# Kernel optimization log

Measured on AMD Instinct MI355X. Metric: run time of the kernel, lower is better.

Reference implementation:

```python
import jax, jax.numpy as jnp
import numpy as np

D_MODEL = 768
N_HEADS = 8
HEAD_DIM = D_MODEL // N_HEADS
B, S, A = 8, 8192, 512


def setup_inputs() -> dict:
    key = jax.random.key(0)
    ks = jax.random.split(key, 12)
    hidden_states = jax.random.normal(ks[0], (B, S, D_MODEL), dtype=jnp.float32)
    # unique anchors per batch element (scatter with duplicates is ill-defined)
    anchor_indices = jax.vmap(lambda k: jax.random.permutation(k, S)[:A])(
        jax.random.split(ks[1], B)).astype(jnp.int64)
    std = 1.0 / np.sqrt(D_MODEL)
    def lin(kw, kb):
        w = jax.random.uniform(kw, (D_MODEL, D_MODEL), jnp.float32, -std, std)
        b = jax.random.uniform(kb, (D_MODEL,), jnp.float32, -std, std)
        return w, b
    wq, bq = lin(ks[2], ks[3])
    wk, bk = lin(ks[4], ks[5])
    wv, bv = lin(ks[6], ks[7])
    wo, bo = lin(ks[8], ks[9])
    ln_g = jnp.ones((D_MODEL,), jnp.float32)
    ln_b = jnp.zeros((D_MODEL,), jnp.float32)
    return dict(hidden_states=hidden_states, anchor_indices=anchor_indices,
                ln_g=ln_g, ln_b=ln_b, wq=wq, bq=bq, wk=wk, bk=bk,
                wv=wv, bv=bv, wo=wo, bo=bo)


def reference(hidden_states, anchor_indices, ln_g, ln_b, wq, bq, wk, bk, wv, bv, wo, bo):
    batch, seq_len, d_model = hidden_states.shape
    n_anchors = anchor_indices.shape[1]
    # gather anchor tokens: (B, A, D)
    anchor_hidden = jnp.take_along_axis(hidden_states, anchor_indices[..., None], axis=1)
    # LayerNorm (eps=1e-5, matching nn.LayerNorm default)
    mu = jnp.mean(anchor_hidden, axis=-1, keepdims=True)
    var = jnp.var(anchor_hidden, axis=-1, keepdims=True)
    x = (anchor_hidden - mu) * jax.lax.rsqrt(var + 1e-5) * ln_g + ln_b
    # QKV projections -> (B, H, A, Hd)
    def heads(y):
        return y.reshape(batch, n_anchors, N_HEADS, HEAD_DIM).transpose(0, 2, 1, 3)
    q = heads(x @ wq.T + bq)
    k = heads(x @ wk.T + bk)
    v = heads(x @ wv.T + bv)
    scale = 1.0 / np.sqrt(HEAD_DIM)
    scores = jnp.einsum('bhad,bhed->bhae', q, k) * scale  # (B,H,A,A)
    attn = jax.nn.softmax(scores, axis=-1)  # dropout is identity in eval
    out = jnp.einsum('bhae,bhed->bhad', attn, v)
    out = out.transpose(0, 2, 1, 3).reshape(batch, n_anchors, d_model)
    out = out @ wo.T + bo
    # scatter back into zeros at anchor positions
    batch_idx = jnp.arange(batch)[:, None]
    output = jnp.zeros_like(hidden_states).at[batch_idx, anchor_indices].set(out)
    return output
```

## Files before the change

kernel.cpp:

```cpp
#include <hip/hip_runtime.h>

#define DM 768
#define NHEAD 8
#define HDIM 96
#define NB 8
#define SEQ 8192
#define NA 512
#define MROW (NB*NA)
#define NQKV (3*DM)
#define QBLK 32
#define FILLB 512

typedef __attribute__((ext_vector_type(4))) float f32x4;
typedef __attribute__((ext_vector_type(8))) short s16x8;

static __device__ __forceinline__ unsigned short f2bf(float x) {
  unsigned int u = __float_as_uint(x);
  u += 0x7fffu + ((u >> 16) & 1u);
  return (unsigned short)(u >> 16);
}
static __device__ __forceinline__ float bf2f(unsigned short h) {
  return __uint_as_float(((unsigned int)h) << 16);
}

static __device__ __forceinline__ void gld_lds16(const void* g, void* l) {
  __builtin_amdgcn_global_load_lds(
      (const __attribute__((address_space(1))) unsigned int*)g,
      (__attribute__((address_space(3))) unsigned int*)l, 16, 0, 0);
}

__global__ __launch_bounds__(256) void prologue(
    const float* __restrict__ hs, const int* __restrict__ anc,
    const float* __restrict__ gam, const float* __restrict__ bet,
    const float* __restrict__ wq, const float* __restrict__ wk,
    const float* __restrict__ wv, const float* __restrict__ wo,
    unsigned short* __restrict__ xh,
    unsigned short* __restrict__ w1h, unsigned short* __restrict__ woh)
{
  __shared__ float red[8];
  const int bid = blockIdx.x;
  const int t = threadIdx.x;
  if (bid < MROW) {
    int r = bid;
    int b = r >> 9, a = r & (NA - 1);
    int idx = anc[b * NA + a];
    const float* src = hs + ((size_t)b * SEQ + idx) * DM;
    float e0 = src[t], e1 = src[t + 256], e2 = src[t + 512];
    float s = e0 + e1 + e2;
    float ss = e0*e0 + e1*e1 + e2*e2;
    #pragma unroll
    for (int o = 1; o < 64; o <<= 1) { s += __shfl_xor(s, o); ss += __shfl_xor(ss, o); }
    int w = t >> 6, lane = t & 63;
    if (lane == 0) { red[w] = s; red[4 + w] = ss; }
    __syncthreads();
    s  = red[0] + red[1] + red[2] + red[3];
    ss = red[4] + red[5] + red[6] + red[7];
    float mu = s * (1.f / DM);
    float var = ss * (1.f / DM) - mu * mu;
    float rstd = rsqrtf(var + 1e-5f);
    size_t base = (size_t)r * DM;
    #pragma unroll
    for (int p = 0; p < 3; ++p) {
      int c = t + p * 256;
      float e = (p == 0) ? e0 : (p == 1) ? e1 : e2;
      float y = (e - mu) * rstd * gam[c] + bet[c];
      xh[base + c] = f2bf(y);
    }
  } else {
    const int i = (bid - MROW) * 256 + t;
    const int T1_4 = (NQKV * DM) / 4;
    const int TW_4 = (DM * DM) / 4;
    float4 v;
    unsigned short* dh; int e4;
    if (i < T1_4) {
      v = (i < TW_4) ? reinterpret_cast<const float4*>(wq)[i]
        : (i < 2*TW_4) ? reinterpret_cast<const float4*>(wk)[i - TW_4]
                       : reinterpret_cast<const float4*>(wv)[i - 2*TW_4];
      dh = w1h; e4 = i;
    } else {
      int j = i - T1_4;
      v = reinterpret_cast<const float4*>(wo)[j];
      dh = woh; e4 = j;
    }
    uint2 ph;
    ph.x = (unsigned)f2bf(v.x) | ((unsigned)f2bf(v.y) << 16);
    ph.y = (unsigned)f2bf(v.z) | ((unsigned)f2bf(v.w) << 16);
    reinterpret_cast<uint2*>(dh)[e4] = ph;
  }
}

template<int EPI>
__global__ __launch_bounds__(256, 4) void gemm128(
    const unsigned short* __restrict__ Ah,
    const unsigned short* __restrict__ Bh,
    const float* __restrict__ biasq, const float* __restrict__ biask, const float* __restrict__ biasv,
    unsigned short* __restrict__ qh,
    unsigned short* __restrict__ kh,
    unsigned short* __restrict__ vh,
    const float* __restrict__ biaso, const int* __restrict__ anc,
    float* __restrict__ outp,
    f32x4* __restrict__ fillp, int n4, int nCompute, int gcols)
{
  __shared__ unsigned short sA[128 * 64], sB[128 * 64];
  const int bidx = blockIdx.x;
  if (bidx >= nCompute) {
    const f32x4 z = {0.f, 0.f, 0.f, 0.f};
    int i = (bidx - nCompute) * 256 + threadIdx.x;
    for (; i < n4; i += FILLB * 256) __builtin_nontemporal_store(z, fillp + i);
    return;
  }
  const int tid = threadIdx.x, lane = tid & 63, w = tid >> 6;
  const int wr = w >> 1, wc = w & 1;
  const unsigned int wg = ((unsigned)bidx & 7) * ((unsigned)nCompute >> 3) + ((unsigned)bidx >> 3);
  const int m0 = (int)(wg / gcols) * 128, n0 = (int)(wg % gcols) * 128;
  const int rsel = lane & 15, kg = lane >> 4;
  f32x4 acc[4][4] = {};

  for (int k0 = 0; k0 < DM; k0 += 64) {
    __syncthreads();
    #pragma unroll
    for (int c = 0; c < 4; ++c) {
      const int gg = w * 256 + c * 64;
      const int g = gg + lane;
      const int row = g >> 3, slot = g & 7;
      const int kk = k0 + ((slot ^ (row & 7)) << 3);
      gld_lds16(Ah + (size_t)(m0 + row) * DM + kk, sA + gg * 8);
      gld_lds16(Bh + (size_t)(n0 + row) * DM + kk, sB + gg * 8);
    }
    __syncthreads();
    #pragma unroll
    for (int s = 0; s < 2; ++s) {
      s16x8 af[4], bf[4];
      #pragma unroll
      for (int i = 0; i < 4; ++i) {
        const int row = wr * 64 + i * 16 + rsel;
        const int as = (((s << 2) | kg) ^ (row & 7));
        af[i] = *reinterpret_cast<const s16x8*>(sA + row * 64 + as * 8);
        const int col = wc * 64 + i * 16 + rsel;
        const int bs = (((s << 2) | kg) ^ (col & 7));
        bf[i] = *reinterpret_cast<const s16x8*>(sB + col * 64 + bs * 8);
      }
      #pragma unroll
      for (int i = 0; i < 4; ++i)
        #pragma unroll
        for (int j = 0; j < 4; ++j)
          acc[i][j] = __builtin_amdgcn_mfma_f32_16x16x32_bf16(af[i], bf[j], acc[i][j], 0, 0, 0);
    }
  }

  #pragma unroll
  for (int i = 0; i < 4; ++i)
    #pragma unroll
    for (int j = 0; j < 4; ++j)
      #pragma unroll
      for (int r = 0; r < 4; ++r) {
        const int row = m0 + wr * 64 + i * 16 + kg * 4 + r;
        const int col = n0 + wc * 64 + j * 16 + rsel;
        const float v = acc[i][j][r];
        const int b = row >> 9, a = row & (NA - 1);
        if (EPI == 1) {
          const int sec = (col >= 2 * DM) ? 2 : (col >= DM ? 1 : 0);
          const int f = col - sec * DM;
          const int hh = f / HDIM, d = f - hh * HDIM;
          const float* bp = (sec == 0) ? biasq : (sec == 1) ? biask : biasv;
          const float val = v + bp[f];
          const int bhh = b * NHEAD + hh;
          if (sec == 0) {
            const size_t o = ((size_t)bhh * NA + a) * HDIM + d; qh[o] = f2bf(val);
          } else if (sec == 1) {
            const size_t o = ((size_t)bhh * NA + a) * HDIM + d; kh[o] = f2bf(val);
          } else {
            const size_t o = ((size_t)bhh * HDIM + d) * NA + a; vh[o] = f2bf(val);
          }
        } else {
          const int sidx = anc[b * NA + a];
          outp[((size_t)b * SEQ + sidx) * DM + col] = v + biaso[col];
        }
      }
}

__global__ __launch_bounds__(512, 4) void attn_fused(
    const unsigned short* __restrict__ qh,
    const unsigned short* __restrict__ kh,
    const unsigned short* __restrict__ vh,
    unsigned short* __restrict__ oh)
{
  __shared__ unsigned int S[QBLK * 512];
  __shared__ float rsum_lds[QBLK];
  const int blk = blockIdx.x;
  const int xcd = blk & 7, slot = blk >> 3;
  const int qt = slot & 15, bh = (slot >> 4) * 8 + xcd;
  const int b = bh >> 3, h = bh & 7;
  const int tid = threadIdx.x, lane = tid & 63, w = tid >> 6;
  const int rt = w & 1, ctq = w >> 1;
  const int rsel = lane & 15, kg = lane >> 4;
  const int q0 = qt * QBLK;

  s16x8 qf[3];
  {
    const size_t qrow = (size_t)bh * NA + q0 + rt * 16 + rsel;
    const unsigned short* qp = qh + qrow * HDIM + kg * 8;
    #pragma unroll
    for (int kc = 0; kc < 3; ++kc)
      qf[kc] = *reinterpret_cast<const s16x8*>(qp + kc * 32);
  }
  const float scale = 0.10206207261596575f;
  const unsigned short* kb_h = kh + (size_t)bh * NA * HDIM;

  for (int ct2 = 0; ct2 < 8; ++ct2) {
    const int ct = ctq * 8 + ct2;
    f32x4 acc = {0.f, 0.f, 0.f, 0.f};
    const unsigned short* kp = kb_h + (size_t)(ct * 16 + rsel) * HDIM + kg * 8;
    #pragma unroll
    for (int kc = 0; kc < 3; ++kc) {
      s16x8 kfh = *reinterpret_cast<const s16x8*>(kp + kc * 32);
      __builtin_amdgcn_s_setprio(1);
      acc = __builtin_amdgcn_mfma_f32_16x16x32_bf16(qf[kc], kfh, acc, 0, 0, 0);
      __builtin_amdgcn_s_setprio(0);
    }
    #pragma unroll
    for (int r = 0; r < 4; ++r) {
      int row = rt * 16 + kg * 4 + r;
      int col = ct * 16 + rsel;
      S[row * 512 + (col ^ ((row & 7) << 2))] = __float_as_uint(acc[r] * scale);
    }
  }
  __syncthreads();

  {
    const int row = w * 4 + (lane >> 4);
    const int sub = lane & 15;
    const int srow = (row & 7) << 2;
    unsigned int* rowp = &S[row * 512];
    float mx = -3.0e38f;
    #pragma unroll 8
    for (int i = 0; i < 8; ++i) {
      int c = sub * 4 + i * 64;
      uint4 u = *reinterpret_cast<const uint4*>(rowp + (c ^ srow));
      mx = fmaxf(mx, fmaxf(fmaxf(__uint_as_float(u.x), __uint_as_float(u.y)),
                           fmaxf(__uint_as_float(u.z), __uint_as_float(u.w))));
    }
    mx = fmaxf(mx, __shfl_xor(mx, 1));
    mx = fmaxf(mx, __shfl_xor(mx, 2));
    mx = fmaxf(mx, __shfl_xor(mx, 4));
    mx = fmaxf(mx, __shfl_xor(mx, 8));
    float sum = 0.f;
    #pragma unroll 8
    for (int i = 0; i < 8; ++i) {
      int c = sub * 4 + i * 64;
      uint4 u = *reinterpret_cast<const uint4*>(rowp + (c ^ srow));
      float p0 = __expf(__uint_as_float(u.x) - mx);
      float p1 = __expf(__uint_as_float(u.y) - mx);
      float p2 = __expf(__uint_as_float(u.z) - mx);
      float p3 = __expf(__uint_as_float(u.w) - mx);
      sum += p0 + p1 + p2 + p3;
      uint4 pk;
      pk.x = ((unsigned)f2bf(p0)) << 16;
      pk.y = ((unsigned)f2bf(p1)) << 16;
      pk.z = ((unsigned)f2bf(p2)) << 16;
      pk.w = ((unsigned)f2bf(p3)) << 16;
      *reinterpret_cast<uint4*>(rowp + (c ^ srow)) = pk;
    }
    sum += __shfl_xor(sum, 1);
    sum += __shfl_xor(sum, 2);
    sum += __shfl_xor(sum, 4);
    sum += __shfl_xor(sum, 8);
    if (sub == 0) rsum_lds[row] = 1.f / sum;
  }
  __syncthreads();

  const unsigned short* vb_h = vh + (size_t)bh * HDIM * NA;
  for (int task = w; task < 12; task += 8) {
    const int nt = task % 6, rt2 = task / 6;
    f32x4 acc = {0.f, 0.f, 0.f, 0.f};
    const int row = rt2 * 16 + rsel;
    const int srow = (row & 7) << 2;
    const unsigned int* rowp = &S[row * 512];
    for (int kc = 0; kc < 16; ++kc) {
      int c = kc * 32 + kg * 8;
      uint4 ua = *reinterpret_cast<const uint4*>(rowp + ((c) ^ srow));
      uint4 ub = *reinterpret_cast<const uint4*>(rowp + ((c + 4) ^ srow));
      s16x8 ph;
      ph[0] = (short)(ua.x >> 16); ph[1] = (short)(ua.y >> 16);
      ph[2] = (short)(ua.z >> 16); ph[3] = (short)(ua.w >> 16);
      ph[4] = (short)(ub.x >> 16); ph[5] = (short)(ub.y >> 16);
      ph[6] = (short)(ub.z >> 16); ph[7] = (short)(ub.w >> 16);
      const unsigned short* vp = vb_h + (size_t)(nt * 16 + rsel) * NA + c;
      s16x8 vfh = *reinterpret_cast<const s16x8*>(vp);
      __builtin_amdgcn_s_setprio(1);
      acc = __builtin_amdgcn_mfma_f32_16x16x32_bf16(ph, vfh, acc, 0, 0, 0);
      __builtin_amdgcn_s_setprio(0);
    }
    #pragma unroll
    for (int r = 0; r < 4; ++r) {
      const float rinv = rsum_lds[rt2 * 16 + kg * 4 + r];
      const int rowg = b * NA + q0 + rt2 * 16 + kg * 4 + r;
      size_t o = (size_t)rowg * DM + h * HDIM + nt * 16 + rsel;
      oh[o] = f2bf(acc[r] * rinv);
    }
  }
}

extern "C" void kernel_launch(void* const* d_in, const int* in_sizes, int n_in,
                              void* d_out, int out_size, void* d_ws, size_t ws_size,
                              hipStream_t stream)
{
  const float* hs   = (const float*)d_in[0];
  const int*   anc  = (const int*)d_in[1];
  const float* ln_g = (const float*)d_in[2];
  const float* ln_b = (const float*)d_in[3];
  const float* wq = (const float*)d_in[4];
  const float* bq = (const float*)d_in[5];
  const float* wk = (const float*)d_in[6];
  const float* bk = (const float*)d_in[7];
  const float* wv = (const float*)d_in[8];
  const float* bv = (const float*)d_in[9];
  const float* wo = (const float*)d_in[10];
  const float* bo = (const float*)d_in[11];
  float* outp = (float*)d_out;

  char* ws = (char*)d_ws;
  size_t off = 0;
  auto take = [&](size_t bytes) { char* p = ws + off; off += (bytes + 255) & ~(size_t)255; return p; };
  unsigned short* xh  = (unsigned short*)take((size_t)MROW * DM * 2);
  unsigned short* w1h = (unsigned short*)take((size_t)NQKV * DM * 2);
  unsigned short* woh = (unsigned short*)take((size_t)DM * DM * 2);
  const size_t qkvsz = (size_t)NB * NHEAD * NA * HDIM * 2;
  unsigned short* qhb = (unsigned short*)take(qkvsz);
  unsigned short* khb = (unsigned short*)take(qkvsz);
  unsigned short* vhb = (unsigned short*)take(qkvsz);
  unsigned short* ohb = (unsigned short*)take((size_t)MROW * DM * 2);

  prologue<<<MROW + 2304, 256, 0, stream>>>(
      hs, anc, ln_g, ln_b, wq, wk, wv, wo, xh, w1h, woh);
  gemm128<1><<<(MROW / 128) * (NQKV / 128) + FILLB, 256, 0, stream>>>(
      xh, w1h, bq, bk, bv, qhb, khb, vhb,
      nullptr, nullptr, nullptr,
      (f32x4*)outp, out_size / 4, (MROW / 128) * (NQKV / 128), NQKV / 128);
  attn_fused<<<NB * NHEAD * (NA / QBLK), 512, 0, stream>>>(
      qhb, khb, vhb, ohb);
  gemm128<2><<<(MROW / 128) * (DM / 128), 256, 0, stream>>>(
      ohb, woh, nullptr, nullptr, nullptr,
      nullptr, nullptr, nullptr,
      bo, anc, outp,
      nullptr, 0, (MROW / 128) * (DM / 128), DM / 128);
}
```

Baseline: 117.8 us.

## Retile GEMMs to 128x96/64x96 and split output zero-fill across GEMM and attention

```diff
diff --git a/kernel.cpp b/kernel.cpp
--- a/kernel.cpp
+++ b/kernel.cpp
@@ -9,7 +9,9 @@
 #define MROW (NB*NA)
 #define NQKV (3*DM)
 #define QBLK 32
-#define FILLB 512
+#define ATTNB 1024
+#define AFILLB 512
+#define GFILLB 512
 
 typedef __attribute__((ext_vector_type(4))) float f32x4;
 typedef __attribute__((ext_vector_type(8))) short s16x8;
@@ -18,9 +20,6 @@
   unsigned int u = __float_as_uint(x);
   u += 0x7fffu + ((u >> 16) & 1u);
   return (unsigned short)(u >> 16);
-}
-static __device__ __forceinline__ float bf2f(unsigned short h) {
-  return __uint_as_float(((unsigned int)h) << 16);
 }
 
 static __device__ __forceinline__ void gld_lds16(const void* g, void* l) {
@@ -89,8 +88,8 @@
   }
 }
 
-template<int EPI>
-__global__ __launch_bounds__(256, 4) void gemm128(
+template<int EPI, int BM, int BN, int NCOMP, int GCOLS>
+__global__ __launch_bounds__(256, 4) void gemm_t(
     const unsigned short* __restrict__ Ah,
     const unsigned short* __restrict__ Bh,
     const float* __restrict__ biasq, const float* __restrict__ biask, const float* __restrict__ biasv,
@@ -99,63 +98,73 @@
     unsigned short* __restrict__ vh,
     const float* __restrict__ biaso, const int* __restrict__ anc,
     float* __restrict__ outp,
-    f32x4* __restrict__ fillp, int n4, int nCompute, int gcols)
+    f32x4* __restrict__ fillp, int fstart, int fend, int nfillb)
 {
-  __shared__ unsigned short sA[128 * 64], sB[128 * 64];
+  constexpr int MI = BM / 32, NJ = BN / 32;
+  __shared__ unsigned short sA[BM * 64], sB[BN * 64];
   const int bidx = blockIdx.x;
-  if (bidx >= nCompute) {
+  if (bidx >= NCOMP) {
     const f32x4 z = {0.f, 0.f, 0.f, 0.f};
-    int i = (bidx - nCompute) * 256 + threadIdx.x;
-    for (; i < n4; i += FILLB * 256) __builtin_nontemporal_store(z, fillp + i);
+    int i = fstart + (bidx - NCOMP) * 256 + threadIdx.x;
+    for (; i < fend; i += nfillb * 256) __builtin_nontemporal_store(z, fillp + i);
     return;
   }
   const int tid = threadIdx.x, lane = tid & 63, w = tid >> 6;
   const int wr = w >> 1, wc = w & 1;
-  const unsigned int wg = ((unsigned)bidx & 7) * ((unsigned)nCompute >> 3) + ((unsigned)bidx >> 3);
-  const int m0 = (int)(wg / gcols) * 128, n0 = (int)(wg % gcols) * 128;
+  const unsigned int wg = ((unsigned)bidx & 7) * (NCOMP >> 3) + ((unsigned)bidx >> 3);
+  const int m0 = (int)(wg / GCOLS) * BM, n0 = (int)(wg % GCOLS) * BN;
   const int rsel = lane & 15, kg = lane >> 4;
-  f32x4 acc[4][4] = {};
+  f32x4 acc[MI][NJ] = {};
 
   for (int k0 = 0; k0 < DM; k0 += 64) {
     __syncthreads();
     #pragma unroll
-    for (int c = 0; c < 4; ++c) {
-      const int gg = w * 256 + c * 64;
+    for (int c = 0; c < (BM + BN) / 32; ++c) {
+      const int gg = c * 256 + w * 64;
       const int g = gg + lane;
-      const int row = g >> 3, slot = g & 7;
-      const int kk = k0 + ((slot ^ (row & 7)) << 3);
-      gld_lds16(Ah + (size_t)(m0 + row) * DM + kk, sA + gg * 8);
-      gld_lds16(Bh + (size_t)(n0 + row) * DM + kk, sB + gg * 8);
+      if (g < BM * 8) {
+        const int row = g >> 3, slot = g & 7;
+        const int kk = k0 + ((slot ^ (row & 7)) << 3);
+        gld_lds16(Ah + (size_t)(m0 + row) * DM + kk, sA + gg * 8);
+      } else {
+        const int g2 = g - BM * 8;
+        const int row = g2 >> 3, slot = g2 & 7;
+        const int kk = k0 + ((slot ^ (row & 7)) << 3);
+        gld_lds16(Bh + (size_t)(n0 + row) * DM + kk, sB + (gg - BM * 8) * 8);
+      }
     }
     __syncthreads();
     #pragma unroll
     for (int s = 0; s < 2; ++s) {
-      s16x8 af[4], bf[4];
+      s16x8 af[MI], bf[NJ];
       #pragma unroll
-      for (int i = 0; i < 4; ++i) {
-        const int row = wr * 64 + i * 16 + rsel;
+      for (int i = 0; i < MI; ++i) {
+        const int row = wr * (MI * 16) + i * 16 + rsel;
         const int as = (((s << 2) | kg) ^ (row & 7));
         af[i] = *reinterpret_cast<const s16x8*>(sA + row * 64 + as * 8);
-        const int col = wc * 64 + i * 16 + rsel;
-        const int bs = (((s << 2) | kg) ^ (col & 7));
-        bf[i] = *reinterpret_cast<const s16x8*>(sB + col * 64 + bs * 8);
       }
       #pragma unroll
-      for (int i = 0; i < 4; ++i)
+      for (int j = 0; j < NJ; ++j) {
+        const int col = wc * (NJ * 16) + j * 16 + rsel;
+        const int bs = (((s << 2) | kg) ^ (col & 7));
+        bf[j] = *reinterpret_cast<const s16x8*>(sB + col * 64 + bs * 8);
+      }
+      #pragma unroll
+      for (int i = 0; i < MI; ++i)
         #pragma unroll
-        for (int j = 0; j < 4; ++j)
+        for (int j = 0; j < NJ; ++j)
           acc[i][j] = __builtin_amdgcn_mfma_f32_16x16x32_bf16(af[i], bf[j], acc[i][j], 0, 0, 0);
     }
   }
 
   #pragma unroll
-  for (int i = 0; i < 4; ++i)
-    #pragma unroll
-    for (int j = 0; j < 4; ++j)
+  for (int i = 0; i < MI; ++i)
+    #pragma unroll
+    for (int j = 0; j < NJ; ++j)
       #pragma unroll
       for (int r = 0; r < 4; ++r) {
-        const int row = m0 + wr * 64 + i * 16 + kg * 4 + r;
-        const int col = n0 + wc * 64 + j * 16 + rsel;
+        const int row = m0 + wr * (MI * 16) + i * 16 + kg * 4 + r;
+        const int col = n0 + wc * (NJ * 16) + j * 16 + rsel;
         const float v = acc[i][j][r];
         const int b = row >> 9, a = row & (NA - 1);
         if (EPI == 1) {
@@ -183,10 +192,17 @@
     const unsigned short* __restrict__ qh,
     const unsigned short* __restrict__ kh,
     const unsigned short* __restrict__ vh,
-    unsigned short* __restrict__ oh)
+    unsigned short* __restrict__ oh,
+    f32x4* __restrict__ fillp, int fstart, int fend)
 {
   __shared__ unsigned int S[QBLK * 512];
   __shared__ float rsum_lds[QBLK];
+  if (blockIdx.x >= ATTNB) {
+    const f32x4 z = {0.f, 0.f, 0.f, 0.f};
+    int i = fstart + (blockIdx.x - ATTNB) * 512 + threadIdx.x;
+    for (; i < fend; i += AFILLB * 512) __builtin_nontemporal_store(z, fillp + i);
+    return;
+  }
   const int blk = blockIdx.x;
   const int xcd = blk & 7, slot = blk >> 3;
   const int qt = slot & 15, bh = (slot >> 4) * 8 + xcd;
@@ -331,17 +347,20 @@
   unsigned short* vhb = (unsigned short*)take(qkvsz);
   unsigned short* ohb = (unsigned short*)take((size_t)MROW * DM * 2);
 
+  const int n4 = out_size / 4;
+  const int fb = (int)(((long long)n4 * 5) / 8);
+
   prologue<<<MROW + 2304, 256, 0, stream>>>(
       hs, anc, ln_g, ln_b, wq, wk, wv, wo, xh, w1h, woh);
-  gemm128<1><<<(MROW / 128) * (NQKV / 128) + FILLB, 256, 0, stream>>>(
+  gemm_t<1, 128, 96, 768, 24><<<768 + GFILLB, 256, 0, stream>>>(
       xh, w1h, bq, bk, bv, qhb, khb, vhb,
       nullptr, nullptr, nullptr,
-      (f32x4*)outp, out_size / 4, (MROW / 128) * (NQKV / 128), NQKV / 128);
-  attn_fused<<<NB * NHEAD * (NA / QBLK), 512, 0, stream>>>(
-      qhb, khb, vhb, ohb);
-  gemm128<2><<<(MROW / 128) * (DM / 128), 256, 0, stream>>>(
+      (f32x4*)outp, 0, fb, GFILLB);
+  attn_fused<<<ATTNB + AFILLB, 512, 0, stream>>>(
+      qhb, khb, vhb, ohb, (f32x4*)outp, fb, n4);
+  gemm_t<2, 64, 96, 512, 8><<<512, 256, 0, stream>>>(
       ohb, woh, nullptr, nullptr, nullptr,
       nullptr, nullptr, nullptr,
       bo, anc, outp,
-      nullptr, 0, (MROW / 128) * (DM / 128), DM / 128);
-}
+      nullptr, 0, 0, 1);
+}
```

Result: faster. 112.6 us (-4.4%).
